# Optimization experiments

Measured on AMD Instinct MI355X. Metric: run time of the kernel, lower is better.

## Reference

```python
import jax, jax.numpy as jnp
import numpy as np
import math

HEADS = 8


def sinusoidal_pe_2d(C, H, W, dtype=jnp.float32):
    """Standard fixed 2D sinusoidal PE. Returns (C, H*W).
    First C/2 channels encode row (H) position, last C/2 encode column (W)."""
    half = C // 2
    div = jnp.exp(-math.log(10000.0) * jnp.arange(0, half, 2, dtype=dtype) / half)  # (half/2,)
    pos_h = jnp.arange(H, dtype=dtype)[:, None] * div[None, :]  # (H, half/2)
    pos_w = jnp.arange(W, dtype=dtype)[:, None] * div[None, :]  # (W, half/2)
    # interleave sin/cos along channel dim -> (H, half), (W, half)
    pe_h = jnp.stack([jnp.sin(pos_h), jnp.cos(pos_h)], axis=-1).reshape(H, half)
    pe_w = jnp.stack([jnp.sin(pos_w), jnp.cos(pos_w)], axis=-1).reshape(W, half)
    pe = jnp.concatenate([
        jnp.broadcast_to(pe_h.T[:, :, None], (half, H, W)),
        jnp.broadcast_to(pe_w.T[:, None, :], (half, H, W)),
    ], axis=0)  # (C, H, W)
    return pe.reshape(C, H * W)


def setup_inputs() -> dict:
    key = jax.random.key(0)
    k1, k2, k3, k4 = jax.random.split(key, 4)
    B, c_in, H, W = 16, 256, 64, 64
    c_out = 512
    s = 1.0 / math.sqrt(c_in)
    return {
        "x": jax.random.normal(k1, (B, c_in, H, W), dtype=jnp.float32),
        "Wq": jax.random.normal(k2, (c_out, c_in), dtype=jnp.float32) * s,
        "Wk": jax.random.normal(k3, (c_out, c_in), dtype=jnp.float32) * s,
        "Wv": jax.random.normal(k4, (c_out, c_in), dtype=jnp.float32) * s,
    }


def reference(x, Wq, Wk, Wv):
    B, C, H, W = x.shape
    M = H * W
    c_out = Wq.shape[0]
    heads = HEADS
    dh = c_out // heads
    scale = 1.0 / math.sqrt(dh)

    xf = x.reshape(B, C, M)
    # 1x1 convs (no bias) == channel matmuls
    q = jnp.einsum('oc,bcm->bom', Wq, xf).reshape(B, heads, dh, M)
    k = jnp.einsum('oc,bcm->bom', Wk, xf).reshape(B, heads, dh, M)
    v = jnp.einsum('oc,bcm->bom', Wv, xf).reshape(B, heads, dh, M)

    r = sinusoidal_pe_2d(c_out, H, W, dtype=x.dtype).reshape(1, heads, dh, M)
    q = (jax.nn.elu(q + r) + 1.0) * scale  # feature map phi(q)
    k = (jax.nn.elu(k) + 1.0) * scale      # feature map phi(k)

    KV = jnp.einsum('bhcm,bhdm->bhcd', k, v)          # (B,h,dh,dh)
    out = jnp.einsum('bhcd,bhcm->bhdm', KV, q)        # (B,h,dh,M)
    k_sum = k.sum(axis=-1)                            # (B,h,dh)
    denom = jnp.einsum('bhcm,bhc->bhm', q, k_sum)
    denom = jnp.maximum(denom, 1e-6)[:, :, None, :]   # (B,h,1,M)
    out = out / denom
    return out.reshape(B, c_out, H, W)
```

## Files before the change

kernel.cpp:

```cpp
#include <hip/hip_runtime.h>

#define NB   16
#define CIN  256
#define MM   4096
#define COUT 512
#define NH   8
#define DH   64
#define SCALE 0.125f

typedef __attribute__((ext_vector_type(8))) short bf16x8;
typedef __attribute__((ext_vector_type(4))) float f32x4;

#define PEH_OFF   0u
#define PEW_OFF   65536u
#define WQ_OFF    131072u
#define WKV_OFF   393216u
#define KVP_OFF   917504u
#define KSP_OFF   9306112u
#define AEXT_OFF  9437184u
#define XT_OFF    27787264u
#define WS_NEED   61341696ull

__device__ __forceinline__ unsigned short f2bf(float f) {
    unsigned int u = __float_as_uint(f);
    u = (u + 0x7FFFu + ((u >> 16) & 1u)) >> 16;
    return (unsigned short)u;
}
__device__ __forceinline__ float phi_elu(float x) {
    return (x >= 0.f ? x + 1.f : __expf(x)) * SCALE;
}
__device__ __forceinline__ void gload_lds16(const void* g, void* l) {
    __builtin_amdgcn_global_load_lds(
        (const __attribute__((address_space(1))) unsigned int*)g,
        (__attribute__((address_space(3))) unsigned int*)l, 16, 0, 0);
}


__global__ __launch_bounds__(256) void k_init(const float* __restrict__ x,
                                              const float* __restrict__ Wq,
                                              const float* __restrict__ Wk,
                                              const float* __restrict__ Wv,
                                              char* __restrict__ ws) {
    __shared__ unsigned short tile[64 * 64];
    int blk = blockIdx.x;
    int t = threadIdx.x;
    if (blk < 1664) {
        int idx = blk * 256 + t;
        if (idx < 32768) {
            int which = idx >> 14;
            int r = idx & 16383;
            int c = r >> 6, pos = r & 63;
            float div = __expf(-logf(10000.f) * (float)(c >> 1) * (1.f / 128.f));
            float tt = (float)pos * div;
            float v = (c & 1) ? cosf(tt) : sinf(tt);
            ((float*)(ws + (which ? PEW_OFF : PEH_OFF)))[r] = v;
            return;
        }
        idx -= 32768;
        if (idx < COUT * CIN) {
            ((unsigned short*)(ws + WQ_OFF))[idx] = f2bf(Wq[idx]);
            return;
        }
        idx -= COUT * CIN;
        if (idx < NH * 128 * CIN) {
            int h = idx >> 15;
            int r = idx & 32767;
            int row = r >> 8, c = r & 255;
// ... 5 lines not shown
    }
    int gx = blk - 1664;
    int ct = gx & 3, mt = (gx >> 2) & 63, b = gx >> 8;
    int m0 = mt * 64, c0 = ct * 64;
    const float* xb = x + ((size_t)b * CIN + c0) * MM + m0;
    int m4 = (t & 15) * 4;
    int cp0 = (t >> 4) * 2;
#pragma unroll
    for (int p = 0; p < 2; ++p) {
        int cp = cp0 + p * 32;
        float4 v0 = *(const float4*)(xb + (size_t)cp * MM + m4);
        float4 v1 = *(const float4*)(xb + (size_t)(cp + 1) * MM + m4);
        float a0[4] = {v0.x, v0.y, v0.z, v0.w};
        float a1[4] = {v1.x, v1.y, v1.z, v1.w};
#pragma unroll
        for (int i = 0; i < 4; ++i) {
            int m = m4 + i;
            unsigned pk = (unsigned)f2bf(a0[i]) | ((unsigned)f2bf(a1[i]) << 16);
            unsigned off = (unsigned)(m * 128) + (((unsigned)(cp * 2)) ^ ((unsigned)(m & 7) << 4));
            *(unsigned*)((char*)tile + off) = pk;
        }
    }
    __syncthreads();
    unsigned short* xt = (unsigned short*)(ws + XT_OFF) + ((size_t)b * MM + m0) * CIN + c0;
#pragma unroll
    for (int p = 0; p < 2; ++p) {
        int id = t + p * 256;
        int m = id >> 3, u = id & 7;
        unsigned off = (unsigned)(m * 128) + (((unsigned)(u ^ (m & 7))) << 4);
        *(bf16x8*)(xt + (size_t)m * CIN + u * 8) = *(const bf16x8*)((const char*)tile + off);
    }
}

__device__ __forceinline__ void stage_half(const unsigned short* __restrict__ tile_base, int h,
                                           unsigned short* __restrict__ buf, int l, int w) {
#pragma unroll
    for (int i = 0; i < 4; ++i) {
        int r0 = w * 16 + i * 4;
        int m = r0 + (l >> 4);
        unsigned u = (unsigned)(l & 15) ^ (unsigned)(m & 7);
        const char* g = (const char*)tile_base + m * 512 + h * 256 + u * 16;
        gload_lds16(g, (char*)buf + r0 * 256);
    }
}
__device__ __forceinline__ bf16x8 ldsBh(const unsigned short* buf, int n, int k) {
    unsigned off = (unsigned)(n * 256) + (((((unsigned)k) >> 3) ^ ((unsigned)n & 7)) << 4);
    return *(const bf16x8*)((const char*)buf + off);
}

__global__ __launch_bounds__(256) void k_kv4(const char* __restrict__ ws) {
    __shared__ unsigned short bufA[64 * 128];
    __shared__ unsigned short bufB[64 * 128];
    __shared__ unsigned short kt[64 * 72];
    __shared__ unsigned short vt[64 * 72];
    int t = threadIdx.x, l = t & 63, w = t >> 6;
    int blk = blockIdx.x;
    int wid = ((blk & 7) << 6) | (blk >> 3);
    int s = wid & 3, bh = wid >> 2;
    int b = bh >> 3, h = bh & 7;
    const unsigned short* xtb = (const unsigned short*)(ws + XT_OFF) + (size_t)b * MM * CIN;
    const unsigned short* wkv = (const unsigned short*)(ws + WKV_OFF) + (size_t)h * 128 * CIN;
    bf16x8 wreg[2][8];
#pragma unroll
    for (int rf = 0; rf < 2; ++rf)
#pragma unroll
        for (int kk = 0; kk < 8; ++kk)
            wreg[rf][kk] = *(const bf16x8*)(wkv + (size_t)(w * 32 + rf * 16 + (l & 15)) * CIN + kk * 32 + (l >> 4) * 8);

    f32x4 kvacc[4] = {};
    float ksum[2][4] = {};

    const unsigned short* tile0 = xtb + (size_t)(s * 1024) * CIN;
    stage_half(tile0, 0, bufA, l, w);
    __syncthreads();

    for (int ms = 0; ms < 16; ++ms) {
        const unsigned short* tilep = xtb + (size_t)(s * 1024 + ms * 64) * CIN;
        stage_half(tilep, 1, bufB, l, w);

        f32x4 acc[2][4] = {};
#pragma unroll
        for (int kk = 0; kk < 4; ++kk) {
            bf16x8 bfr[4];
#pragma unroll
            for (int cf = 0; cf < 4; ++cf)
                bfr[cf] = ldsBh(bufA, cf * 16 + (l & 15), kk * 32 + (l >> 4) * 8);
#pragma unroll
            for (int rf = 0; rf < 2; ++rf)
#pragma unroll
                for (int cf = 0; cf < 4; ++cf)
                    acc[rf][cf] = __builtin_amdgcn_mfma_f32_16x16x32_bf16(wreg[rf][kk], bfr[cf], acc[rf][cf], 0, 0, 0);
        }
        __syncthreads();

        if (ms < 15)
            stage_half(tilep + 64 * CIN, 0, bufA, l, w);
#pragma unroll
        for (int kk = 0; kk < 4; ++kk) {
            bf16x8 bfr[4];
#pragma unroll
            for (int cf = 0; cf < 4; ++cf)
                bfr[cf] = ldsBh(bufB, cf * 16 + (l & 15), kk * 32 + (l >> 4) * 8);
#pragma unroll
            for (int rf = 0; rf < 2; ++rf)
#pragma unroll
                for (int cf = 0; cf < 4; ++cf)
                    acc[rf][cf] = __builtin_amdgcn_mfma_f32_16x16x32_bf16(wreg[rf][4 + kk], bfr[cf], acc[rf][cf], 0, 0, 0);
        }
        if (w < 2) {
#pragma unroll
            for (int rf = 0; rf < 2; ++rf)
#pragma unroll
                for (int cf = 0; cf < 4; ++cf)
#pragma unroll
                    for (int r = 0; r < 4; ++r) {
                        float p = phi_elu(acc[rf][cf][r]);
                        ksum[rf][r] += p;
                        kt[(w * 32 + rf * 16 + ((l >> 4) << 2) + r) * 72 + cf * 16 + (l & 15)] = f2bf(p);
                    }
        } else {
#pragma unroll
            for (int rf = 0; rf < 2; ++rf)
#pragma unroll
                for (int cf = 0; cf < 4; ++cf)
#pragma unroll
                    for (int r = 0; r < 4; ++r)
                        vt[((w - 2) * 32 + rf * 16 + ((l >> 4) << 2) + r) * 72 + cf * 16 + (l & 15)] = f2bf(acc[rf][cf][r]);
        }
        __syncthreads();
#pragma unroll
        for (int kk = 0; kk < 2; ++kk) {
            bf16x8 a = *(const bf16x8*)(kt + (w * 16 + (l & 15)) * 72 + kk * 32 + (l >> 4) * 8);
#pragma unroll
            for (int cf = 0; cf < 4; ++cf) {
                bf16x8 bb = *(const bf16x8*)(vt + (cf * 16 + (l & 15)) * 72 + kk * 32 + (l >> 4) * 8);
                kvacc[cf] = __builtin_amdgcn_mfma_f32_16x16x32_bf16(a, bb, kvacc[cf], 0, 0, 0);
            }
        }
    }

    float* kvp = (float*)(ws + KVP_OFF) + ((size_t)(bh * 4 + s)) * 4096;
#pragma unroll
    for (int cf = 0; cf < 4; ++cf)
#pragma unroll
        for (int r = 0; r < 4; ++r) {
            int c = w * 16 + ((l >> 4) << 2) + r;
            kvp[c * 64 + cf * 16 + (l & 15)] = kvacc[cf][r];
        }
    if (w < 2) {
        float* ksp = (float*)(ws + KSP_OFF) + (bh * 4 + s) * 64;
#pragma unroll
        for (int rf = 0; rf < 2; ++rf)
#pragma unroll
            for (int r = 0; r < 4; ++r) {
                float v = ksum[rf][r];
                v += __shfl_xor(v, 1); v += __shfl_xor(v, 2);
                v += __shfl_xor(v, 4); v += __shfl_xor(v, 8);
                if ((l & 15) == 0)
                    ksp[w * 32 + rf * 16 + ((l >> 4) << 2) + r] = v;
            }
    }
}

__global__ __launch_bounds__(256) void k_out4(const char* __restrict__ ws, float* __restrict__ out) {
    __shared__ unsigned short bufA[64 * 128];
    __shared__ unsigned short bufB[64 * 128];
    __shared__ unsigned short qt[64 * 64];
    __shared__ unsigned short aext[80 * 72];
    int t = threadIdx.x, l = t & 63, w = t >> 6;
    int blk = blockIdx.x;
    int wid = ((blk & 7) << 6) | (blk >> 3);
    int chunk = wid & 3, bh = wid >> 2;
    int b = bh >> 3, h = bh & 7;

    {
        const float* kvp = (const float*)(ws + KVP_OFF) + (size_t)bh * 4 * 4096;
        const float* ksp = (const float*)(ws + KSP_OFF) + bh * 4 * 64;
        for (int j = t; j < 4096; j += 256) {
            float v = kvp[j] + kvp[4096 + j] + kvp[8192 + j] + kvp[12288 + j];
            aext[(j & 63) * 72 + (j >> 6)] = f2bf(v);
        }
        if (t < 64) {
            float v = ksp[t] + ksp[64 + t] + ksp[128 + t] + ksp[192 + t];
            aext[64 * 72 + t] = f2bf(v);
        }
        for (int j = t; j < 15 * 64; j += 256)
            aext[(65 + (j >> 6)) * 72 + (j & 63)] = 0;
    }

    const unsigned short* xtb = (const unsigned short*)(ws + XT_OFF) + (size_t)b * MM * CIN;
    const unsigned short* wq = (const unsigned short*)(ws + WQ_OFF);
    bf16x8 wreg[2][8];
#pragma unroll
    for (int rf = 0; rf < 2; ++rf)
#pragma unroll
        for (int kk = 0; kk < 8; ++kk)
            wreg[rf][kk] = *(const bf16x8*)(wq + (size_t)(h * 64 + (w >> 1) * 32 + rf * 16 + (l & 15)) * CIN + kk * 32 + (l >> 4) * 8);

    const float* pe = (h < 4) ? (const float*)(ws + PEH_OFF) : (const float*)(ws + PEW_OFF);
    int obase = h * 64 - (h < 4 ? 0 : 256);
    float* outbh = out + ((size_t)(b * COUT + h * DH)) * MM;

    const unsigned short* tile0 = xtb + (size_t)(chunk * 1024) * CIN;
    stage_half(tile0, 0, bufA, l, w);
    __syncthreads();

    for (int ms = 0; ms < 16; ++ms) {
        int m0 = chunk * 1024 + ms * 64;
        const unsigned short* tilep = xtb + (size_t)m0 * CIN;
        stage_half(tilep, 1, bufB, l, w);

        f32x4 acc[2][2] = {};
#pragma unroll
        for (int kk = 0; kk < 4; ++kk) {
            bf16x8 bfr[2];
#pragma unroll
            for (int mf = 0; mf < 2; ++mf)
                bfr[mf] = ldsBh(bufA, (w & 1) * 32 + mf * 16 + (l & 15), kk * 32 + (l >> 4) * 8);
#pragma unroll
            for (int rf = 0; rf < 2; ++rf)
#pragma unroll
                for (int mf = 0; mf < 2; ++mf)
                    acc[rf][mf] = __builtin_amdgcn_mfma_f32_16x16x32_bf16(wreg[rf][kk], bfr[mf], acc[rf][mf], 0, 0, 0);
        }
        __syncthreads();

        if (ms < 15)
            stage_half(tilep + 64 * CIN, 0, bufA, l, w);
#pragma unroll
        for (int kk = 0; kk < 4; ++kk) {
            bf16x8 bfr[2];
#pragma unroll
            for (int mf = 0; mf < 2; ++mf)
                bfr[mf] = ldsBh(bufB, (w & 1) * 32 + mf * 16 + (l & 15), kk * 32 + (l >> 4) * 8);
#pragma unroll
            for (int rf = 0; rf < 2; ++rf)
#pragma unroll
                for (int mf = 0; mf < 2; ++mf)
                    acc[rf][mf] = __builtin_amdgcn_mfma_f32_16x16x32_bf16(wreg[rf][4 + kk], bfr[mf], acc[rf][mf], 0, 0, 0);
        }
        int im = m0 >> 6;
#pragma unroll
        for (int rf = 0; rf < 2; ++rf) {
#pragma unroll
            for (int mf = 0; mf < 2; ++mf) {
                int mloc = (w & 1) * 32 + mf * 16 + (l & 15);
#pragma unroll
                for (int r = 0; r < 4; ++r) {
                    int c = (w >> 1) * 32 + rf * 16 + ((l >> 4) << 2) + r;
                    int o = obase + c;
                    float pev = (h < 4) ? pe[o * 64 + im] : pe[o * 64 + mloc];
                    float v = phi_elu(acc[rf][mf][r] + pev);
                    unsigned off = (unsigned)(mloc * 128) + (((unsigned)(c * 2)) ^ ((unsigned)(mloc & 7) << 4));
                    *(unsigned short*)((char*)qt + off) = f2bf(v);
                }
            }
        }
        __syncthreads();

        f32x4 acc2[5] = {};
#pragma unroll
        for (int kk = 0; kk < 2; ++kk) {
            int m = w * 16 + (l & 15);
            unsigned koff = (unsigned)(kk * 64 + (l >> 4) * 16);
            unsigned off = (unsigned)(m * 128) + (koff ^ ((unsigned)(m & 7) << 4));
            bf16x8 bb = *(const bf16x8*)((const char*)qt + off);
#pragma unroll
            for (int rf = 0; rf < 5; ++rf) {
                bf16x8 a = *(const bf16x8*)(aext + (rf * 16 + (l & 15)) * 72 + kk * 32 + (l >> 4) * 8);
                acc2[rf] = __builtin_amdgcn_mfma_f32_16x16x32_bf16(a, bb, acc2[rf], 0, 0, 0);
            }
        }
        float den = __shfl(acc2[4][0], l & 15);
        float inv = 1.f / fmaxf(den, 1e-6f);
        int mcol = m0 + w * 16 + (l & 15);
#pragma unroll
        for (int rf = 0; rf < 4; ++rf)
#pragma unroll
            for (int r = 0; r < 4; ++r)
                outbh[(size_t)(rf * 16 + ((l >> 4) << 2) + r) * MM + mcol] = acc2[rf][r] * inv;
    }
}


__global__ void k_prep(const float* __restrict__ Wq, const float* __restrict__ Wk,
                       const float* __restrict__ Wv, char* __restrict__ ws) {
    int idx = blockIdx.x * 256 + threadIdx.x;
    if (idx < 32768) {
        int which = idx >> 14;
        int r = idx & 16383;
        int c = r >> 6, pos = r & 63;
        float div = __expf(-logf(10000.f) * (float)(c >> 1) * (1.f / 128.f));
        float t = (float)pos * div;
        float v = (c & 1) ? cosf(t) : sinf(t);
        ((float*)(ws + (which ? PEW_OFF : PEH_OFF)))[r] = v;
        return;
    }
    idx -= 32768;
    if (idx < COUT * CIN) {
        ((unsigned short*)(ws + WQ_OFF))[idx] = f2bf(Wq[idx]);
        return;
    }
    idx -= COUT * CIN;
    if (idx < NH * 128 * CIN) {
        int h = idx >> 15;
        int r = idx & 32767;
        int row = r >> 8, c = r & 255;
        float v = (row < 64) ? Wk[(h * 64 + row) * CIN + c]
                             : Wv[(h * 64 + row - 64) * CIN + c];
        ((unsigned short*)(ws + WKV_OFF))[idx] = f2bf(v);
    }
}

// ... 119 lines not shown
        if (w < 2) {
#pragma unroll
            for (int rf = 0; rf < 2; ++rf)
#pragma unroll
                for (int cf = 0; cf < 4; ++cf)
#pragma unroll
                    for (int r = 0; r < 4; ++r) {
                        float p = phi_elu(acc[rf][cf][r]);
                        ksum[rf][r] += p;
                        kt[(w * 32 + rf * 16 + ((l >> 4) << 2) + r) * 72 + cf * 16 + (l & 15)] = f2bf(p);
                    }
        } else {
#pragma unroll
            for (int rf = 0; rf < 2; ++rf)
#pragma unroll
                for (int cf = 0; cf < 4; ++cf)
#pragma unroll
                    for (int r = 0; r < 4; ++r)
                        vt[((w - 2) * 32 + rf * 16 + ((l >> 4) << 2) + r) * 72 + cf * 16 + (l & 15)] = f2bf(acc[rf][cf][r]);
        }
        __syncthreads();

#pragma unroll
        for (int kk = 0; kk < 2; ++kk) {
            bf16x8 a = *(const bf16x8*)(kt + (w * 16 + (l & 15)) * 72 + kk * 32 + (l >> 4) * 8);
#pragma unroll
            for (int cf = 0; cf < 4; ++cf) {
                bf16x8 bb = *(const bf16x8*)(vt + (cf * 16 + (l & 15)) * 72 + kk * 32 + (l >> 4) * 8);
                kvacc[cf] = __builtin_amdgcn_mfma_f32_16x16x32_bf16(a, bb, kvacc[cf], 0, 0, 0);
            }
        }
    }

    float* kvp = (float*)(ws + KVP_OFF) + ((size_t)(bh * 4 + s)) * 64 * 64;
#pragma unroll
    for (int cf = 0; cf < 4; ++cf)
#pragma unroll
        for (int r = 0; r < 4; ++r) {
            int c = w * 16 + ((l >> 4) << 2) + r;
            kvp[c * 64 + cf * 16 + (l & 15)] = kvacc[cf][r];
        }
    if (w < 2) {
        float* ksp = (float*)(ws + KSP_OFF) + (bh * 4 + s) * 64;
#pragma unroll
        for (int rf = 0; rf < 2; ++rf)
#pragma unroll
            for (int r = 0; r < 4; ++r) {
                float v = ksum[rf][r];
                v += __shfl_xor(v, 1); v += __shfl_xor(v, 2);
                v += __shfl_xor(v, 4); v += __shfl_xor(v, 8);
                if ((l & 15) == 0)
                    ksp[w * 32 + rf * 16 + ((l >> 4) << 2) + r] = v;
            }
    }
}

__global__ void k_reduce(char* __restrict__ ws) {
    int bh = blockIdx.x;
    const float* kvp = (const float*)(ws + KVP_OFF) + (size_t)bh * 4 * 4096;
    const float* ksp = (const float*)(ws + KSP_OFF) + bh * 4 * 64;
    unsigned short* a = (unsigned short*)(ws + AEXT_OFF) + (size_t)bh * 80 * 64;
    for (int i = threadIdx.x; i < 80 * 64; i += 256) {
        int d = i >> 6, c = i & 63;
        float v = 0.f;
        if (d < 64) {
#pragma unroll
            for (int s = 0; s < 4; ++s) v += kvp[s * 4096 + c * 64 + d];
// ... 36 lines not shown
        __syncthreads();
        f32x4 acc[5] = {};
#pragma unroll
        for (int kk = 0; kk < 2; ++kk) {
            bf16x8 bb = *(const bf16x8*)(qt + (w * 16 + (l & 15)) * 72 + kk * 32 + (l >> 4) * 8);
#pragma unroll
            for (int rf = 0; rf < 5; ++rf) {
                bf16x8 a = *(const bf16x8*)(aext + (rf * 16 + (l & 15)) * 72 + kk * 32 + (l >> 4) * 8);
                acc[rf] = __builtin_amdgcn_mfma_f32_16x16x32_bf16(a, bb, acc[rf], 0, 0, 0);
            }
        }
        float den = __shfl(acc[4][0], l & 15);
        float inv = 1.f / fmaxf(den, 1e-6f);
        int mcol = m0 + w * 16 + (l & 15);
#pragma unroll
        for (int rf = 0; rf < 4; ++rf)
#pragma unroll
            for (int r = 0; r < 4; ++r)
                outbh[(size_t)(rf * 16 + ((l >> 4) << 2) + r) * MM + mcol] = acc[rf][r] * inv;
    }
}

extern "C" void kernel_launch(void* const* d_in, const int* in_sizes, int n_in,
                              void* d_out, int out_size, void* d_ws, size_t ws_size,
                              hipStream_t stream) {
    const float* x  = (const float*)d_in[0];
    const float* Wq = (const float*)d_in[1];
    const float* Wk = (const float*)d_in[2];
    const float* Wv = (const float*)d_in[3];
    float* out = (float*)d_out;
    char* ws = (char*)d_ws;

    if (ws_size >= WS_NEED) {
        hipLaunchKernelGGL(k_init,  dim3(5760), dim3(256), 0, stream, x, Wq, Wk, Wv, ws);
        hipLaunchKernelGGL(k_kv4,   dim3(512),  dim3(256), 0, stream, ws);
        hipLaunchKernelGGL(k_out4,  dim3(512),  dim3(256), 0, stream, ws, out);
    } else {
        hipLaunchKernelGGL(k_prep,   dim3(1664), dim3(256), 0, stream, Wq, Wk, Wv, ws);
        hipLaunchKernelGGL(k_qgemm,  dim3(2048), dim3(512), 0, stream, x, ws, out);
        hipLaunchKernelGGL(k_kv,     dim3(512),  dim3(256), 0, stream, x, ws);
        hipLaunchKernelGGL(k_reduce, dim3(128),  dim3(256), 0, stream, ws);
        hipLaunchKernelGGL(k_out,    dim3(1024), dim3(256), 0, stream, ws, out);
    }
}
```

Measured before the change: 122.8 us.

## Split M into 8 chunks with quarter-K double-buffered staging in kv/out kernels

The KV and output kernels now split the 4096-position dimension into 8 chunks instead of 4, doubling the grid to 1024 blocks. The LDS staging buffers shrink to a quarter of K per stage, and each stage is double-buffered and prefetched one step ahead, which lowers shared memory per block and allows launch_bounds(256,4) occupancy. The aim is better CU utilisation and overlap of loads with MFMA work. The cost is more partial KV/ksum buffers to reduce in k_out6 and more barriers per tile.

After: 285.2 us. 2.32x slower.

```diff
diff --git a/kernel.cpp b/kernel.cpp
--- a/kernel.cpp
+++ b/kernel.cpp
@@ -18,6 +18,8 @@
 #define KVP_OFF   917504u
 #define KSP_OFF   9306112u
 #define AEXT_OFF  9437184u
+#define KVP8_OFF  9437184u
+#define KSP8_OFF  26214400u
 #define XT_OFF    27787264u
 #define WS_NEED   61341696ull
 
@@ -104,31 +106,31 @@
     }
 }
 
-__device__ __forceinline__ void stage_half(const unsigned short* __restrict__ tile_base, int h,
-                                           unsigned short* __restrict__ buf, int l, int w) {
-#pragma unroll
-    for (int i = 0; i < 4; ++i) {
-        int r0 = w * 16 + i * 4;
-        int m = r0 + (l >> 4);
-        unsigned u = (unsigned)(l & 15) ^ (unsigned)(m & 7);
-        const char* g = (const char*)tile_base + m * 512 + h * 256 + u * 16;
-        gload_lds16(g, (char*)buf + r0 * 256);
-    }
-}
-__device__ __forceinline__ bf16x8 ldsBh(const unsigned short* buf, int n, int k) {
-    unsigned off = (unsigned)(n * 256) + (((((unsigned)k) >> 3) ^ ((unsigned)n & 7)) << 4);
+__device__ __forceinline__ void stage_q(const unsigned short* __restrict__ tile_base, int q,
+                                        unsigned short* __restrict__ buf, int l, int w) {
+#pragma unroll
+    for (int p = 0; p < 2; ++p) {
+        int r0 = w * 16 + p * 8;
+        int m = r0 + (l >> 3);
+        unsigned u = (unsigned)(l & 7) ^ (unsigned)(m & 7);
+        const char* g = (const char*)tile_base + m * 512 + q * 128 + u * 16;
+        gload_lds16(g, (char*)buf + r0 * 128);
+    }
+}
+__device__ __forceinline__ bf16x8 ldsQ(const unsigned short* buf, int n, int k) {
+    unsigned off = (unsigned)(n * 128) + (((((unsigned)k) >> 3) ^ ((unsigned)n & 7)) << 4);
     return *(const bf16x8*)((const char*)buf + off);
 }
 
-__global__ __launch_bounds__(256) void k_kv4(const char* __restrict__ ws) {
-    __shared__ unsigned short bufA[64 * 128];
-    __shared__ unsigned short bufB[64 * 128];
+__global__ __launch_bounds__(256, 4) void k_kv6(const char* __restrict__ ws) {
+    __shared__ unsigned short bufA[64 * 64];
+    __shared__ unsigned short bufB[64 * 64];
     __shared__ unsigned short kt[64 * 72];
     __shared__ unsigned short vt[64 * 72];
     int t = threadIdx.x, l = t & 63, w = t >> 6;
     int blk = blockIdx.x;
-    int wid = ((blk & 7) << 6) | (blk >> 3);
-    int s = wid & 3, bh = wid >> 2;
+    int wid = ((blk & 7) << 7) | (blk >> 3);
+    int s = wid & 7, bh = wid >> 3;
     int b = bh >> 3, h = bh & 7;
     const unsigned short* xtb = (const unsigned short*)(ws + XT_OFF) + (size_t)b * MM * CIN;
     const unsigned short* wkv = (const unsigned short*)(ws + WKV_OFF) + (size_t)h * 128 * CIN;
@@ -141,43 +143,37 @@
 
     f32x4 kvacc[4] = {};
     float ksum[2][4] = {};
-
-    const unsigned short* tile0 = xtb + (size_t)(s * 1024) * CIN;
-    stage_half(tile0, 0, bufA, l, w);
+    unsigned short* bufs[2] = {bufA, bufB};
+
+    const unsigned short* base = xtb + (size_t)(s * 512) * CIN;
+    stage_q(base, 0, bufA, l, w);
     __syncthreads();
 
-    for (int ms = 0; ms < 16; ++ms) {
-        const unsigned short* tilep = xtb + (size_t)(s * 1024 + ms * 64) * CIN;
-        stage_half(tilep, 1, bufB, l, w);
-
+    for (int ms = 0; ms < 8; ++ms) {
+        const unsigned short* tilep = base + (size_t)(ms * 64) * CIN;
         f32x4 acc[2][4] = {};
 #pragma unroll
-        for (int kk = 0; kk < 4; ++kk) {
-            bf16x8 bfr[4];
-#pragma unroll
-            for (int cf = 0; cf < 4; ++cf)
-                bfr[cf] = ldsBh(bufA, cf * 16 + (l & 15), kk * 32 + (l >> 4) * 8);
-#pragma unroll
-            for (int rf = 0; rf < 2; ++rf)
+        for (int q = 0; q < 4; ++q) {
+            int g = ms * 4 + q;
+            if (g + 1 < 32) {
+                const unsigned short* tn = base + (size_t)(((g + 1) >> 2) * 64) * CIN;
+                stage_q(tn, (g + 1) & 3, bufs[(g + 1) & 1], l, w);
+            }
+            const unsigned short* cur = bufs[g & 1];
+#pragma unroll
+            for (int kl = 0; kl < 2; ++kl) {
+                int kk = q * 2 + kl;
+                bf16x8 bfr[4];
 #pragma unroll
                 for (int cf = 0; cf < 4; ++cf)
-                    acc[rf][cf] = __builtin_amdgcn_mfma_f32_16x16x32_bf16(wreg[rf][kk], bfr[cf], acc[rf][cf], 0, 0, 0);
-        }
-        __syncthreads();
-
-        if (ms < 15)
-            stage_half(tilep + 64 * CIN, 0, bufA, l, w);
-#pragma unroll
-        for (int kk = 0; kk < 4; ++kk) {
-            bf16x8 bfr[4];
-#pragma unroll
-            for (int cf = 0; cf < 4; ++cf)
-                bfr[cf] = ldsBh(bufB, cf * 16 + (l & 15), kk * 32 + (l >> 4) * 8);
-#pragma unroll
-            for (int rf = 0; rf < 2; ++rf)
-#pragma unroll
-                for (int cf = 0; cf < 4; ++cf)
-                    acc[rf][cf] = __builtin_amdgcn_mfma_f32_16x16x32_bf16(wreg[rf][4 + kk], bfr[cf], acc[rf][cf], 0, 0, 0);
+                    bfr[cf] = ldsQ(cur, cf * 16 + (l & 15), kl * 32 + (l >> 4) * 8);
+#pragma unroll
+                for (int rf = 0; rf < 2; ++rf)
+#pragma unroll
+                    for (int cf = 0; cf < 4; ++cf)
+                        acc[rf][cf] = __builtin_amdgcn_mfma_f32_16x16x32_bf16(wreg[rf][kk], bfr[cf], acc[rf][cf], 0, 0, 0);
+            }
+            __syncthreads();
         }
         if (w < 2) {
 #pragma unroll
@@ -211,7 +207,7 @@
         }
     }
 
-    float* kvp = (float*)(ws + KVP_OFF) + ((size_t)(bh * 4 + s)) * 4096;
+    float* kvp = (float*)(ws + KVP8_OFF) + ((size_t)(bh * 8 + s)) * 4096;
 #pragma unroll
     for (int cf = 0; cf < 4; ++cf)
 #pragma unroll
@@ -220,7 +216,7 @@
             kvp[c * 64 + cf * 16 + (l & 15)] = kvacc[cf][r];
         }
     if (w < 2) {
-        float* ksp = (float*)(ws + KSP_OFF) + (bh * 4 + s) * 64;
+        float* ksp = (float*)(ws + KSP8_OFF) + (bh * 8 + s) * 64;
 #pragma unroll
         for (int rf = 0; rf < 2; ++rf)
 #pragma unroll
@@ -234,26 +230,30 @@
     }
 }
 
-__global__ __launch_bounds__(256) void k_out4(const char* __restrict__ ws, float* __restrict__ out) {
-    __shared__ unsigned short bufA[64 * 128];
-    __shared__ unsigned short bufB[64 * 128];
+__global__ __launch_bounds__(256, 4) void k_out6(const char* __restrict__ ws, float* __restrict__ out) {
+    __shared__ unsigned short bufA[64 * 64];
+    __shared__ unsigned short bufB[64 * 64];
     __shared__ unsigned short qt[64 * 64];
     __shared__ unsigned short aext[80 * 72];
     int t = threadIdx.x, l = t & 63, w = t >> 6;
     int blk = blockIdx.x;
-    int wid = ((blk & 7) << 6) | (blk >> 3);
-    int chunk = wid & 3, bh = wid >> 2;
+    int wid = ((blk & 7) << 7) | (blk >> 3);
+    int chunk = wid & 7, bh = wid >> 3;
     int b = bh >> 3, h = bh & 7;
 
     {
-        const float* kvp = (const float*)(ws + KVP_OFF) + (size_t)bh * 4 * 4096;
-        const float* ksp = (const float*)(ws + KSP_OFF) + bh * 4 * 64;
+        const float* kvp = (const float*)(ws + KVP8_OFF) + (size_t)bh * 8 * 4096;
+        const float* ksp = (const float*)(ws + KSP8_OFF) + bh * 8 * 64;
         for (int j = t; j < 4096; j += 256) {
-            float v = kvp[j] + kvp[4096 + j] + kvp[8192 + j] + kvp[12288 + j];
+            float v = 0.f;
+#pragma unroll
+            for (int sx = 0; sx < 8; ++sx) v += kvp[sx * 4096 + j];
             aext[(j & 63) * 72 + (j >> 6)] = f2bf(v);
         }
         if (t < 64) {
-            float v = ksp[t] + ksp[64 + t] + ksp[128 + t] + ksp[192 + t];
+            float v = 0.f;
+#pragma unroll
+            for (int sx = 0; sx < 8; ++sx) v += ksp[sx * 64 + t];
             aext[64 * 72 + t] = f2bf(v);
         }
         for (int j = t; j < 15 * 64; j += 256)
@@ -272,44 +272,37 @@
     const float* pe = (h < 4) ? (const float*)(ws + PEH_OFF) : (const float*)(ws + PEW_OFF);
     int obase = h * 64 - (h < 4 ? 0 : 256);
     float* outbh = out + ((size_t)(b * COUT + h * DH)) * MM;
-
-    const unsigned short* tile0 = xtb + (size_t)(chunk * 1024) * CIN;
-    stage_half(tile0, 0, bufA, l, w);
+    unsigned short* bufs[2] = {bufA, bufB};
+
+    const unsigned short* base = xtb + (size_t)(chunk * 512) * CIN;
+    stage_q(base, 0, bufA, l, w);
     __syncthreads();
 
-    for (int ms = 0; ms < 16; ++ms) {
-        int m0 = chunk * 1024 + ms * 64;
-        const unsigned short* tilep = xtb + (size_t)m0 * CIN;
-        stage_half(tilep, 1, bufB, l, w);
-
+    for (int ms = 0; ms < 8; ++ms) {
+        int m0 = chunk * 512 + ms * 64;
         f32x4 acc[2][2] = {};
 #pragma unroll
-        for (int kk = 0; kk < 4; ++kk) {
-            bf16x8 bfr[2];
-#pragma unroll
-            for (int mf = 0; mf < 2; ++mf)
-                bfr[mf] = ldsBh(bufA, (w & 1) * 32 + mf * 16 + (l & 15), kk * 32 + (l >> 4) * 8);
-#pragma unroll
-            for (int rf = 0; rf < 2; ++rf)
+        for (int q = 0; q < 4; ++q) {
+            int g = ms * 4 + q;
+            if (g + 1 < 32) {
+                const unsigned short* tn = base + (size_t)(((g + 1) >> 2) * 64) * CIN;
+                stage_q(tn, (g + 1) & 3, bufs[(g + 1) & 1], l, w);
+            }
+            const unsigned short* cur = bufs[g & 1];
+#pragma unroll
+            for (int kl = 0; kl < 2; ++kl) {
+                int kk = q * 2 + kl;
+                bf16x8 bfr[2];
 #pragma unroll
                 for (int mf = 0; mf < 2; ++mf)
-                    acc[rf][mf] = __builtin_amdgcn_mfma_f32_16x16x32_bf16(wreg[rf][kk], bfr[mf], acc[rf][mf], 0, 0, 0);
-        }
-        __syncthreads();
-
-        if (ms < 15)
-            stage_half(tilep + 64 * CIN, 0, bufA, l, w);
-#pragma unroll
-        for (int kk = 0; kk < 4; ++kk) {
-            bf16x8 bfr[2];
-#pragma unroll
-            for (int mf = 0; mf < 2; ++mf)
-                bfr[mf] = ldsBh(bufB, (w & 1) * 32 + mf * 16 + (l & 15), kk * 32 + (l >> 4) * 8);
-#pragma unroll
-            for (int rf = 0; rf < 2; ++rf)
-#pragma unroll
-                for (int mf = 0; mf < 2; ++mf)
-                    acc[rf][mf] = __builtin_amdgcn_mfma_f32_16x16x32_bf16(wreg[rf][4 + kk], bfr[mf], acc[rf][mf], 0, 0, 0);
+                    bfr[mf] = ldsQ(cur, (w & 1) * 32 + mf * 16 + (l & 15), kl * 32 + (l >> 4) * 8);
+#pragma unroll
+                for (int rf = 0; rf < 2; ++rf)
+#pragma unroll
+                    for (int mf = 0; mf < 2; ++mf)
+                        acc[rf][mf] = __builtin_amdgcn_mfma_f32_16x16x32_bf16(wreg[rf][kk], bfr[mf], acc[rf][mf], 0, 0, 0);
+            }
+            __syncthreads();
         }
         int im = m0 >> 6;
 #pragma unroll
@@ -536,7 +529,7 @@
         }
     }
 
-    float* kvp = (float*)(ws + KVP_OFF) + ((size_t)(bh * 4 + s)) * 64 * 64;
+    float* kvp = (float*)(ws + KVP_OFF) + ((size_t)(bh * 4 + s)) * 4096;
 #pragma unroll
     for (int cf = 0; cf < 4; ++cf)
 #pragma unroll
@@ -639,9 +632,9 @@
     char* ws = (char*)d_ws;
 
     if (ws_size >= WS_NEED) {
-        hipLaunchKernelGGL(k_init,  dim3(5760), dim3(256), 0, stream, x, Wq, Wk, Wv, ws);
-        hipLaunchKernelGGL(k_kv4,   dim3(512),  dim3(256), 0, stream, ws);
-        hipLaunchKernelGGL(k_out4,  dim3(512),  dim3(256), 0, stream, ws, out);
+        hipLaunchKernelGGL(k_init, dim3(5760), dim3(256), 0, stream, x, Wq, Wk, Wv, ws);
+        hipLaunchKernelGGL(k_kv6,  dim3(1024), dim3(256), 0, stream, ws);
+        hipLaunchKernelGGL(k_out6, dim3(1024), dim3(256), 0, stream, ws, out);
     } else {
         hipLaunchKernelGGL(k_prep,   dim3(1664), dim3(256), 0, stream, Wq, Wk, Wv, ws);
         hipLaunchKernelGGL(k_qgemm,  dim3(2048), dim3(512), 0, stream, x, ws, out);
```

## Triple-buffer x tiles with fine-grained vmcnt waits in kv and out kernels

Applied to the files above, without the earlier changes.

Replaces the double-buffered LDS staging in k_kv4 and k_out4 with a rotating triple buffer. Each half-tile is issued one stage earlier, and __syncthreads is replaced by explicit s_waitcnt vmcnt/lgkmcnt plus s_barrier, so global-to-LDS loads stay in flight across barriers instead of being drained. The goal is to hide x-tile load latency behind the MFMA work. It costs an extra 16KB of LDS per block, which may lower occupancy, and relies on hand-counted vmcnt values being correct.

Result: slower. 130.8 us (+6.5%).

```diff
diff --git a/kernel.cpp b/kernel.cpp
--- a/kernel.cpp
+++ b/kernel.cpp
@@ -33,6 +33,21 @@
     __builtin_amdgcn_global_load_lds(
         (const __attribute__((address_space(1))) unsigned int*)g,
         (__attribute__((address_space(3))) unsigned int*)l, 16, 0, 0);
+}
+__device__ __forceinline__ void wait_vm4_bar() {
+    asm volatile("s_waitcnt vmcnt(4)" ::: "memory");
+    __builtin_amdgcn_s_barrier();
+    __builtin_amdgcn_sched_barrier(0);
+}
+__device__ __forceinline__ void wait_vm0_bar() {
+    asm volatile("s_waitcnt vmcnt(0)" ::: "memory");
+    __builtin_amdgcn_s_barrier();
+    __builtin_amdgcn_sched_barrier(0);
+}
+__device__ __forceinline__ void wait_lgkm_bar() {
+    asm volatile("s_waitcnt lgkmcnt(0)" ::: "memory");
+    __builtin_amdgcn_s_barrier();
+    __builtin_amdgcn_sched_barrier(0);
 }
 
 
@@ -121,8 +136,9 @@
 }
 
 __global__ __launch_bounds__(256) void k_kv4(const char* __restrict__ ws) {
-    __shared__ unsigned short bufA[64 * 128];
-    __shared__ unsigned short bufB[64 * 128];
+    __shared__ unsigned short b0[64 * 128];
+    __shared__ unsigned short b1[64 * 128];
+    __shared__ unsigned short b2[64 * 128];
     __shared__ unsigned short kt[64 * 72];
     __shared__ unsigned short vt[64 * 72];
     int t = threadIdx.x, l = t & 63, w = t >> 6;
@@ -142,37 +158,36 @@
     f32x4 kvacc[4] = {};
     float ksum[2][4] = {};
 
-    const unsigned short* tile0 = xtb + (size_t)(s * 1024) * CIN;
-    stage_half(tile0, 0, bufA, l, w);
-    __syncthreads();
+    const unsigned short* base = xtb + (size_t)(s * 1024) * CIN;
+    stage_half(base, 0, b0, l, w);
+    stage_half(base, 1, b1, l, w);
+    unsigned short *X = b0, *Y = b1, *Z = b2;
 
     for (int ms = 0; ms < 16; ++ms) {
-        const unsigned short* tilep = xtb + (size_t)(s * 1024 + ms * 64) * CIN;
-        stage_half(tilep, 1, bufB, l, w);
-
+        const unsigned short* tn = base + (size_t)((ms + 1) * 64) * CIN;
+        wait_vm4_bar();
+        if (ms < 15) stage_half(tn, 0, Z, l, w);
         f32x4 acc[2][4] = {};
 #pragma unroll
         for (int kk = 0; kk < 4; ++kk) {
             bf16x8 bfr[4];
 #pragma unroll
             for (int cf = 0; cf < 4; ++cf)
-                bfr[cf] = ldsBh(bufA, cf * 16 + (l & 15), kk * 32 + (l >> 4) * 8);
+                bfr[cf] = ldsBh(X, cf * 16 + (l & 15), kk * 32 + (l >> 4) * 8);
 #pragma unroll
             for (int rf = 0; rf < 2; ++rf)
 #pragma unroll
                 for (int cf = 0; cf < 4; ++cf)
                     acc[rf][cf] = __builtin_amdgcn_mfma_f32_16x16x32_bf16(wreg[rf][kk], bfr[cf], acc[rf][cf], 0, 0, 0);
         }
-        __syncthreads();
-
-        if (ms < 15)
-            stage_half(tilep + 64 * CIN, 0, bufA, l, w);
+        if (ms < 15) wait_vm4_bar(); else wait_vm0_bar();
+        if (ms < 15) stage_half(tn, 1, X, l, w);
 #pragma unroll
         for (int kk = 0; kk < 4; ++kk) {
             bf16x8 bfr[4];
 #pragma unroll
             for (int cf = 0; cf < 4; ++cf)
-                bfr[cf] = ldsBh(bufB, cf * 16 + (l & 15), kk * 32 + (l >> 4) * 8);
+                bfr[cf] = ldsBh(Y, cf * 16 + (l & 15), kk * 32 + (l >> 4) * 8);
 #pragma unroll
             for (int rf = 0; rf < 2; ++rf)
 #pragma unroll
@@ -199,7 +214,7 @@
                     for (int r = 0; r < 4; ++r)
                         vt[((w - 2) * 32 + rf * 16 + ((l >> 4) << 2) + r) * 72 + cf * 16 + (l & 15)] = f2bf(acc[rf][cf][r]);
         }
-        __syncthreads();
+        wait_lgkm_bar();
 #pragma unroll
         for (int kk = 0; kk < 2; ++kk) {
             bf16x8 a = *(const bf16x8*)(kt + (w * 16 + (l & 15)) * 72 + kk * 32 + (l >> 4) * 8);
@@ -209,6 +224,8 @@
                 kvacc[cf] = __builtin_amdgcn_mfma_f32_16x16x32_bf16(a, bb, kvacc[cf], 0, 0, 0);
             }
         }
+        unsigned short* oX = X; unsigned short* oY = Y;
+        X = Z; Y = oX; Z = oY;
     }
 
     float* kvp = (float*)(ws + KVP_OFF) + ((size_t)(bh * 4 + s)) * 4096;
@@ -235,8 +252,9 @@
 }
 
 __global__ __launch_bounds__(256) void k_out4(const char* __restrict__ ws, float* __restrict__ out) {
-    __shared__ unsigned short bufA[64 * 128];
-    __shared__ unsigned short bufB[64 * 128];
+    __shared__ unsigned short b0[64 * 128];
+    __shared__ unsigned short b1[64 * 128];
+    __shared__ unsigned short b2[64 * 128];
     __shared__ unsigned short qt[64 * 64];
     __shared__ unsigned short aext[80 * 72];
     int t = threadIdx.x, l = t & 63, w = t >> 6;
@@ -273,38 +291,38 @@
     int obase = h * 64 - (h < 4 ? 0 : 256);
     float* outbh = out + ((size_t)(b * COUT + h * DH)) * MM;
 
-    const unsigned short* tile0 = xtb + (size_t)(chunk * 1024) * CIN;
-    stage_half(tile0, 0, bufA, l, w);
-    __syncthreads();
+    const unsigned short* base = xtb + (size_t)(chunk * 1024) * CIN;
+    stage_half(base, 0, b0, l, w);
+    stage_half(base, 1, b1, l, w);
+    wait_lgkm_bar();
+    unsigned short *X = b0, *Y = b1, *Z = b2;
 
     for (int ms = 0; ms < 16; ++ms) {
         int m0 = chunk * 1024 + ms * 64;
-        const unsigned short* tilep = xtb + (size_t)m0 * CIN;
-        stage_half(tilep, 1, bufB, l, w);
-
+        const unsigned short* tn = base + (size_t)((ms + 1) * 64) * CIN;
+        wait_vm4_bar();
+        if (ms < 15) stage_half(tn, 0, Z, l, w);
         f32x4 acc[2][2] = {};
 #pragma unroll
         for (int kk = 0; kk < 4; ++kk) {
             bf16x8 bfr[2];
 #pragma unroll
             for (int mf = 0; mf < 2; ++mf)
-                bfr[mf] = ldsBh(bufA, (w & 1) * 32 + mf * 16 + (l & 15), kk * 32 + (l >> 4) * 8);
+                bfr[mf] = ldsBh(X, (w & 1) * 32 + mf * 16 + (l & 15), kk * 32 + (l >> 4) * 8);
 #pragma unroll
             for (int rf = 0; rf < 2; ++rf)
 #pragma unroll
                 for (int mf = 0; mf < 2; ++mf)
                     acc[rf][mf] = __builtin_amdgcn_mfma_f32_16x16x32_bf16(wreg[rf][kk], bfr[mf], acc[rf][mf], 0, 0, 0);
         }
-        __syncthreads();
-
-        if (ms < 15)
-            stage_half(tilep + 64 * CIN, 0, bufA, l, w);
+        if (ms < 15) wait_vm4_bar(); else wait_vm0_bar();
+        if (ms < 15) stage_half(tn, 1, X, l, w);
 #pragma unroll
         for (int kk = 0; kk < 4; ++kk) {
             bf16x8 bfr[2];
 #pragma unroll
             for (int mf = 0; mf < 2; ++mf)
-                bfr[mf] = ldsBh(bufB, (w & 1) * 32 + mf * 16 + (l & 15), kk * 32 + (l >> 4) * 8);
+                bfr[mf] = ldsBh(Y, (w & 1) * 32 + mf * 16 + (l & 15), kk * 32 + (l >> 4) * 8);
 #pragma unroll
             for (int rf = 0; rf < 2; ++rf)
 #pragma unroll
@@ -328,7 +346,7 @@
                 }
             }
         }
-        __syncthreads();
+        wait_lgkm_bar();
 
         f32x4 acc2[5] = {};
 #pragma unroll
@@ -351,6 +369,8 @@
 #pragma unroll
             for (int r = 0; r < 4; ++r)
                 outbh[(size_t)(rf * 16 + ((l >> 4) << 2) + r) * MM + mcol] = acc2[rf][r] * inv;
+        unsigned short* oX = X; unsigned short* oY = Y;
+        X = Z; Y = oX; Z = oY;
     }
 }
 
@@ -536,7 +556,7 @@
         }
     }
 
-    float* kvp = (float*)(ws + KVP_OFF) + ((size_t)(bh * 4 + s)) * 64 * 64;
+    float* kvp = (float*)(ws + KVP_OFF) + ((size_t)(bh * 4 + s)) * 4096;
 #pragma unroll
     for (int cf = 0; cf < 4; ++cf)
 #pragma unroll
@@ -639,9 +659,9 @@
     char* ws = (char*)d_ws;
 
     if (ws_size >= WS_NEED) {
-        hipLaunchKernelGGL(k_init,  dim3(5760), dim3(256), 0, stream, x, Wq, Wk, Wv, ws);
-        hipLaunchKernelGGL(k_kv4,   dim3(512),  dim3(256), 0, stream, ws);
-        hipLaunchKernelGGL(k_out4,  dim3(512),  dim3(256), 0, stream, ws, out);
+        hipLaunchKernelGGL(k_init, dim3(5760), dim3(256), 0, stream, x, Wq, Wk, Wv, ws);
+        hipLaunchKernelGGL(k_kv4,  dim3(512),  dim3(256), 0, stream, ws);
+        hipLaunchKernelGGL(k_out4, dim3(512),  dim3(256), 0, stream, ws, out);
     } else {
         hipLaunchKernelGGL(k_prep,   dim3(1664), dim3(256), 0, stream, Wq, Wk, Wv, ws);
         hipLaunchKernelGGL(k_qgemm,  dim3(2048), dim3(512), 0, stream, x, ws, out);
```

## Keep phi(k) and phi(q) in registers as MFMA operands, skipping LDS round trip

Applied to the files above, without the earlier changes.

Both the KV and output kernels now arrange the projection GEMM so that each wave's accumulator layout matches the operand layout needed by the following MFMA. phi(k) and phi(q) are packed to bf16 in registers and fed directly into the second matmul, which removes the kt/qt shared-memory staging and one barrier in the output kernel. The KV kernel splits the work per wave differently: each wave computes K and V for 16 channels instead of waves specialising on K or V, and the k-sum reduction is simplified. The trade-off is more weight registers in k_out7 (4x8 bf16x8), which could lower occupancy, and 8-byte-split LDS reads of V and aext.

Result: slower. 167.6 us (+36.5%).

```diff
diff --git a/kernel.cpp b/kernel.cpp
--- a/kernel.cpp
+++ b/kernel.cpp
@@ -9,6 +9,7 @@
 #define SCALE 0.125f
 
 typedef __attribute__((ext_vector_type(8))) short bf16x8;
+typedef __attribute__((ext_vector_type(4))) short bf16x4;
 typedef __attribute__((ext_vector_type(4))) float f32x4;
 
 #define PEH_OFF   0u
@@ -33,6 +34,12 @@
     __builtin_amdgcn_global_load_lds(
         (const __attribute__((address_space(1))) unsigned int*)g,
         (__attribute__((address_space(3))) unsigned int*)l, 16, 0, 0);
+}
+__device__ __forceinline__ bf16x8 cat8(bf16x4 a, bf16x4 b) {
+    bf16x8 r;
+    r[0] = a[0]; r[1] = a[1]; r[2] = a[2]; r[3] = a[3];
+    r[4] = b[0]; r[5] = b[1]; r[6] = b[2]; r[7] = b[3];
+    return r;
 }
 
 
@@ -120,10 +127,9 @@
     return *(const bf16x8*)((const char*)buf + off);
 }
 
-__global__ __launch_bounds__(256) void k_kv4(const char* __restrict__ ws) {
+__global__ __launch_bounds__(256) void k_kv7(const char* __restrict__ ws) {
     __shared__ unsigned short bufA[64 * 128];
     __shared__ unsigned short bufB[64 * 128];
-    __shared__ unsigned short kt[64 * 72];
     __shared__ unsigned short vt[64 * 72];
     int t = threadIdx.x, l = t & 63, w = t >> 6;
     int blk = blockIdx.x;
@@ -137,31 +143,31 @@
     for (int rf = 0; rf < 2; ++rf)
 #pragma unroll
         for (int kk = 0; kk < 8; ++kk)
-            wreg[rf][kk] = *(const bf16x8*)(wkv + (size_t)(w * 32 + rf * 16 + (l & 15)) * CIN + kk * 32 + (l >> 4) * 8);
+            wreg[rf][kk] = *(const bf16x8*)(wkv + (size_t)(rf * 64 + w * 16 + (l & 15)) * CIN + kk * 32 + (l >> 4) * 8);
 
     f32x4 kvacc[4] = {};
-    float ksum[2][4] = {};
-
-    const unsigned short* tile0 = xtb + (size_t)(s * 1024) * CIN;
-    stage_half(tile0, 0, bufA, l, w);
+    float ksum_run = 0.f;
+
+    const unsigned short* base = xtb + (size_t)(s * 1024) * CIN;
+    stage_half(base, 0, bufA, l, w);
     __syncthreads();
 
     for (int ms = 0; ms < 16; ++ms) {
-        const unsigned short* tilep = xtb + (size_t)(s * 1024 + ms * 64) * CIN;
+        const unsigned short* tilep = base + (size_t)(ms * 64) * CIN;
         stage_half(tilep, 1, bufB, l, w);
 
-        f32x4 acc[2][4] = {};
+        f32x4 acc[4][2] = {};
 #pragma unroll
         for (int kk = 0; kk < 4; ++kk) {
-            bf16x8 bfr[4];
-#pragma unroll
-            for (int cf = 0; cf < 4; ++cf)
-                bfr[cf] = ldsBh(bufA, cf * 16 + (l & 15), kk * 32 + (l >> 4) * 8);
-#pragma unroll
-            for (int rf = 0; rf < 2; ++rf)
-#pragma unroll
-                for (int cf = 0; cf < 4; ++cf)
-                    acc[rf][cf] = __builtin_amdgcn_mfma_f32_16x16x32_bf16(wreg[rf][kk], bfr[cf], acc[rf][cf], 0, 0, 0);
+            bf16x8 xf[4];
+#pragma unroll
+            for (int mf = 0; mf < 4; ++mf)
+                xf[mf] = ldsBh(bufA, mf * 16 + (l & 15), kk * 32 + (l >> 4) * 8);
+#pragma unroll
+            for (int mf = 0; mf < 4; ++mf)
+#pragma unroll
+                for (int rf = 0; rf < 2; ++rf)
+                    acc[mf][rf] = __builtin_amdgcn_mfma_f32_16x16x32_bf16(xf[mf], wreg[rf][kk], acc[mf][rf], 0, 0, 0);
         }
         __syncthreads();
 
@@ -169,75 +175,62 @@
             stage_half(tilep + 64 * CIN, 0, bufA, l, w);
 #pragma unroll
         for (int kk = 0; kk < 4; ++kk) {
-            bf16x8 bfr[4];
-#pragma unroll
-            for (int cf = 0; cf < 4; ++cf)
-                bfr[cf] = ldsBh(bufB, cf * 16 + (l & 15), kk * 32 + (l >> 4) * 8);
-#pragma unroll
-            for (int rf = 0; rf < 2; ++rf)
-#pragma unroll
-                for (int cf = 0; cf < 4; ++cf)
-                    acc[rf][cf] = __builtin_amdgcn_mfma_f32_16x16x32_bf16(wreg[rf][4 + kk], bfr[cf], acc[rf][cf], 0, 0, 0);
-        }
-        if (w < 2) {
-#pragma unroll
-            for (int rf = 0; rf < 2; ++rf)
-#pragma unroll
-                for (int cf = 0; cf < 4; ++cf)
-#pragma unroll
-                    for (int r = 0; r < 4; ++r) {
-                        float p = phi_elu(acc[rf][cf][r]);
-                        ksum[rf][r] += p;
-                        kt[(w * 32 + rf * 16 + ((l >> 4) << 2) + r) * 72 + cf * 16 + (l & 15)] = f2bf(p);
-                    }
-        } else {
-#pragma unroll
-            for (int rf = 0; rf < 2; ++rf)
-#pragma unroll
-                for (int cf = 0; cf < 4; ++cf)
-#pragma unroll
-                    for (int r = 0; r < 4; ++r)
-                        vt[((w - 2) * 32 + rf * 16 + ((l >> 4) << 2) + r) * 72 + cf * 16 + (l & 15)] = f2bf(acc[rf][cf][r]);
+            bf16x8 xf[4];
+#pragma unroll
+            for (int mf = 0; mf < 4; ++mf)
+                xf[mf] = ldsBh(bufB, mf * 16 + (l & 15), kk * 32 + (l >> 4) * 8);
+#pragma unroll
+            for (int mf = 0; mf < 4; ++mf)
+#pragma unroll
+                for (int rf = 0; rf < 2; ++rf)
+                    acc[mf][rf] = __builtin_amdgcn_mfma_f32_16x16x32_bf16(xf[mf], wreg[rf][4 + kk], acc[mf][rf], 0, 0, 0);
+        }
+        bf16x4 phik[4];
+#pragma unroll
+        for (int mf = 0; mf < 4; ++mf) {
+            bf16x4 pk, pv;
+#pragma unroll
+            for (int r = 0; r < 4; ++r) {
+                float p = phi_elu(acc[mf][0][r]);
+                ksum_run += p;
+                pk[r] = (short)f2bf(p);
+                pv[r] = (short)f2bf(acc[mf][1][r]);
+            }
+            phik[mf] = pk;
+            *(bf16x4*)(vt + (w * 16 + (l & 15)) * 72 + mf * 16 + (l >> 4) * 4) = pv;
         }
         __syncthreads();
 #pragma unroll
-        for (int kk = 0; kk < 2; ++kk) {
-            bf16x8 a = *(const bf16x8*)(kt + (w * 16 + (l & 15)) * 72 + kk * 32 + (l >> 4) * 8);
-#pragma unroll
-            for (int cf = 0; cf < 4; ++cf) {
-                bf16x8 bb = *(const bf16x8*)(vt + (cf * 16 + (l & 15)) * 72 + kk * 32 + (l >> 4) * 8);
-                kvacc[cf] = __builtin_amdgcn_mfma_f32_16x16x32_bf16(a, bb, kvacc[cf], 0, 0, 0);
+        for (int ks = 0; ks < 2; ++ks) {
+            bf16x8 A = cat8(phik[2 * ks], phik[2 * ks + 1]);
+#pragma unroll
+            for (int di = 0; di < 4; ++di) {
+                const unsigned short* vr = vt + (di * 16 + (l & 15)) * 72 + ks * 32 + (l >> 4) * 4;
+                bf16x8 B = cat8(*(const bf16x4*)vr, *(const bf16x4*)(vr + 16));
+                kvacc[di] = __builtin_amdgcn_mfma_f32_16x16x32_bf16(A, B, kvacc[di], 0, 0, 0);
             }
         }
     }
 
     float* kvp = (float*)(ws + KVP_OFF) + ((size_t)(bh * 4 + s)) * 4096;
 #pragma unroll
-    for (int cf = 0; cf < 4; ++cf)
+    for (int di = 0; di < 4; ++di)
 #pragma unroll
         for (int r = 0; r < 4; ++r) {
             int c = w * 16 + ((l >> 4) << 2) + r;
-            kvp[c * 64 + cf * 16 + (l & 15)] = kvacc[cf][r];
-        }
-    if (w < 2) {
+            kvp[c * 64 + di * 16 + (l & 15)] = kvacc[di][r];
+        }
+    {
         float* ksp = (float*)(ws + KSP_OFF) + (bh * 4 + s) * 64;
-#pragma unroll
-        for (int rf = 0; rf < 2; ++rf)
-#pragma unroll
-            for (int r = 0; r < 4; ++r) {
-                float v = ksum[rf][r];
-                v += __shfl_xor(v, 1); v += __shfl_xor(v, 2);
-                v += __shfl_xor(v, 4); v += __shfl_xor(v, 8);
-                if ((l & 15) == 0)
-                    ksp[w * 32 + rf * 16 + ((l >> 4) << 2) + r] = v;
-            }
-    }
-}
-
-__global__ __launch_bounds__(256) void k_out4(const char* __restrict__ ws, float* __restrict__ out) {
+        float v = ksum_run;
+        v += __shfl_xor(v, 16); v += __shfl_xor(v, 32);
+        if (l < 16) ksp[w * 16 + l] = v;
+    }
+}
+
+__global__ __launch_bounds__(256) void k_out7(const char* __restrict__ ws, float* __restrict__ out) {
     __shared__ unsigned short bufA[64 * 128];
     __shared__ unsigned short bufB[64 * 128];
-    __shared__ unsigned short qt[64 * 64];
     __shared__ unsigned short aext[80 * 72];
     int t = threadIdx.x, l = t & 63, w = t >> 6;
     int blk = blockIdx.x;
@@ -262,19 +255,19 @@
 
     const unsigned short* xtb = (const unsigned short*)(ws + XT_OFF) + (size_t)b * MM * CIN;
     const unsigned short* wq = (const unsigned short*)(ws + WQ_OFF);
-    bf16x8 wreg[2][8];
-#pragma unroll
-    for (int rf = 0; rf < 2; ++rf)
+    bf16x8 wreg[4][8];
+#pragma unroll
+    for (int rf = 0; rf < 4; ++rf)
 #pragma unroll
         for (int kk = 0; kk < 8; ++kk)
-            wreg[rf][kk] = *(const bf16x8*)(wq + (size_t)(h * 64 + (w >> 1) * 32 + rf * 16 + (l & 15)) * CIN + kk * 32 + (l >> 4) * 8);
+            wreg[rf][kk] = *(const bf16x8*)(wq + (size_t)(h * 64 + rf * 16 + (l & 15)) * CIN + kk * 32 + (l >> 4) * 8);
 
     const float* pe = (h < 4) ? (const float*)(ws + PEH_OFF) : (const float*)(ws + PEW_OFF);
     int obase = h * 64 - (h < 4 ? 0 : 256);
     float* outbh = out + ((size_t)(b * COUT + h * DH)) * MM;
 
-    const unsigned short* tile0 = xtb + (size_t)(chunk * 1024) * CIN;
-    stage_half(tile0, 0, bufA, l, w);
+    const unsigned short* base = xtb + (size_t)(chunk * 1024) * CIN;
+    stage_half(base, 0, bufA, l, w);
     __syncthreads();
 
     for (int ms = 0; ms < 16; ++ms) {
@@ -282,18 +275,13 @@
         const unsigned short* tilep = xtb + (size_t)m0 * CIN;
         stage_half(tilep, 1, bufB, l, w);
 
-        f32x4 acc[2][2] = {};
+        f32x4 qacc[4] = {};
 #pragma unroll
         for (int kk = 0; kk < 4; ++kk) {
-            bf16x8 bfr[2];
-#pragma unroll
-            for (int mf = 0; mf < 2; ++mf)
-                bfr[mf] = ldsBh(bufA, (w & 1) * 32 + mf * 16 + (l & 15), kk * 32 + (l >> 4) * 8);
-#pragma unroll
-            for (int rf = 0; rf < 2; ++rf)
-#pragma unroll
-                for (int mf = 0; mf < 2; ++mf)
-                    acc[rf][mf] = __builtin_amdgcn_mfma_f32_16x16x32_bf16(wreg[rf][kk], bfr[mf], acc[rf][mf], 0, 0, 0);
+            bf16x8 xf = ldsBh(bufA, w * 16 + (l & 15), kk * 32 + (l >> 4) * 8);
+#pragma unroll
+            for (int rf = 0; rf < 4; ++rf)
+                qacc[rf] = __builtin_amdgcn_mfma_f32_16x16x32_bf16(wreg[rf][kk], xf, qacc[rf], 0, 0, 0);
         }
         __syncthreads();
 
@@ -301,56 +289,45 @@
             stage_half(tilep + 64 * CIN, 0, bufA, l, w);
 #pragma unroll
         for (int kk = 0; kk < 4; ++kk) {
-            bf16x8 bfr[2];
-#pragma unroll
-            for (int mf = 0; mf < 2; ++mf)
-                bfr[mf] = ldsBh(bufB, (w & 1) * 32 + mf * 16 + (l & 15), kk * 32 + (l >> 4) * 8);
-#pragma unroll
-            for (int rf = 0; rf < 2; ++rf)
-#pragma unroll
-                for (int mf = 0; mf < 2; ++mf)
-                    acc[rf][mf] = __builtin_amdgcn_mfma_f32_16x16x32_bf16(wreg[rf][4 + kk], bfr[mf], acc[rf][mf], 0, 0, 0);
+            bf16x8 xf = ldsBh(bufB, w * 16 + (l & 15), kk * 32 + (l >> 4) * 8);
+#pragma unroll
+            for (int rf = 0; rf < 4; ++rf)
+                qacc[rf] = __builtin_amdgcn_mfma_f32_16x16x32_bf16(wreg[rf][4 + kk], xf, qacc[rf], 0, 0, 0);
         }
         int im = m0 >> 6;
-#pragma unroll
-        for (int rf = 0; rf < 2; ++rf) {
-#pragma unroll
-            for (int mf = 0; mf < 2; ++mf) {
-                int mloc = (w & 1) * 32 + mf * 16 + (l & 15);
-#pragma unroll
-                for (int r = 0; r < 4; ++r) {
-                    int c = (w >> 1) * 32 + rf * 16 + ((l >> 4) << 2) + r;
-                    int o = obase + c;
-                    float pev = (h < 4) ? pe[o * 64 + im] : pe[o * 64 + mloc];
-                    float v = phi_elu(acc[rf][mf][r] + pev);
-                    unsigned off = (unsigned)(mloc * 128) + (((unsigned)(c * 2)) ^ ((unsigned)(mloc & 7) << 4));
-                    *(unsigned short*)((char*)qt + off) = f2bf(v);
-                }
-            }
-        }
-        __syncthreads();
-
+        int mloc = w * 16 + (l & 15);
+        bf16x4 qbf[4];
+#pragma unroll
+        for (int rf = 0; rf < 4; ++rf) {
+            bf16x4 qv;
+#pragma unroll
+            for (int r = 0; r < 4; ++r) {
+                int c = rf * 16 + ((l >> 4) << 2) + r;
+                int o = obase + c;
+                float pev = (h < 4) ? pe[o * 64 + im] : pe[o * 64 + mloc];
+                qv[r] = (short)f2bf(phi_elu(qacc[rf][r] + pev));
+            }
+            qbf[rf] = qv;
+        }
         f32x4 acc2[5] = {};
 #pragma unroll
-        for (int kk = 0; kk < 2; ++kk) {
-            int m = w * 16 + (l & 15);
-            unsigned koff = (unsigned)(kk * 64 + (l >> 4) * 16);
-            unsigned off = (unsigned)(m * 128) + (koff ^ ((unsigned)(m & 7) << 4));
-            bf16x8 bb = *(const bf16x8*)((const char*)qt + off);
-#pragma unroll
-            for (int rf = 0; rf < 5; ++rf) {
-                bf16x8 a = *(const bf16x8*)(aext + (rf * 16 + (l & 15)) * 72 + kk * 32 + (l >> 4) * 8);
-                acc2[rf] = __builtin_amdgcn_mfma_f32_16x16x32_bf16(a, bb, acc2[rf], 0, 0, 0);
+        for (int ks = 0; ks < 2; ++ks) {
+            bf16x8 B = cat8(qbf[2 * ks], qbf[2 * ks + 1]);
+#pragma unroll
+            for (int arf = 0; arf < 5; ++arf) {
+                const unsigned short* ar = aext + (arf * 16 + (l & 15)) * 72 + ks * 32 + (l >> 4) * 4;
+                bf16x8 A = cat8(*(const bf16x4*)ar, *(const bf16x4*)(ar + 16));
+                acc2[arf] = __builtin_amdgcn_mfma_f32_16x16x32_bf16(A, B, acc2[arf], 0, 0, 0);
             }
         }
         float den = __shfl(acc2[4][0], l & 15);
         float inv = 1.f / fmaxf(den, 1e-6f);
         int mcol = m0 + w * 16 + (l & 15);
 #pragma unroll
-        for (int rf = 0; rf < 4; ++rf)
+        for (int arf = 0; arf < 4; ++arf)
 #pragma unroll
             for (int r = 0; r < 4; ++r)
-                outbh[(size_t)(rf * 16 + ((l >> 4) << 2) + r) * MM + mcol] = acc2[rf][r] * inv;
+                outbh[(size_t)(arf * 16 + ((l >> 4) << 2) + r) * MM + mcol] = acc2[arf][r] * inv;
     }
 }
 
@@ -536,7 +513,7 @@
         }
     }
 
-    float* kvp = (float*)(ws + KVP_OFF) + ((size_t)(bh * 4 + s)) * 64 * 64;
+    float* kvp = (float*)(ws + KVP_OFF) + ((size_t)(bh * 4 + s)) * 4096;
 #pragma unroll
     for (int cf = 0; cf < 4; ++cf)
 #pragma unroll
@@ -639,9 +616,9 @@
     char* ws = (char*)d_ws;
 
     if (ws_size >= WS_NEED) {
-        hipLaunchKernelGGL(k_init,  dim3(5760), dim3(256), 0, stream, x, Wq, Wk, Wv, ws);
-        hipLaunchKernelGGL(k_kv4,   dim3(512),  dim3(256), 0, stream, ws);
-        hipLaunchKernelGGL(k_out4,  dim3(512),  dim3(256), 0, stream, ws, out);
+        hipLaunchKernelGGL(k_init, dim3(5760), dim3(256), 0, stream, x, Wq, Wk, Wv, ws);
+        hipLaunchKernelGGL(k_kv7,  dim3(512),  dim3(256), 0, stream, ws);
+        hipLaunchKernelGGL(k_out7, dim3(512),  dim3(256), 0, stream, ws, out);
     } else {
         hipLaunchKernelGGL(k_prep,   dim3(1664), dim3(256), 0, stream, Wq, Wk, Wv, ws);
         hipLaunchKernelGGL(k_qgemm,  dim3(2048), dim3(512), 0, stream, x, ws, out);
```
